# Performance work log

Hardware: AMD Instinct MI355X
Metric: run time of the kernel (lower is better)

## Reference

```python
import jax, jax.numpy as jnp
import numpy as np

TOP_K = 2

def _expert(x, w1, w2, w3):
    return (jax.nn.silu(x @ w1.T) * (x @ w3.T)) @ w2.T

def setup_inputs() -> dict:
    key = jax.random.key(0)
    ks = jax.random.split(key, 8)
    B, L, D, F, E, S = 4, 2048, 1024, 512, 16, 1
    p = lambda k, shape: (jax.random.normal(k, shape, jnp.float32) * 0.02)
    return {
        "x": jax.random.normal(ks[0], (B, L, D), jnp.float32),
        "gate_w": p(ks[1], (E, D)),
        "expert_bias": jnp.zeros((E,), jnp.float32),
        "sw1": p(ks[2], (S, F, D)),
        "sw2": p(ks[3], (S, D, F)),
        "sw3": p(ks[4], (S, F, D)),
        "ew1": p(ks[5], (E, F, D)),
        "ew2": p(ks[6], (E, D, F)),
        "ew3": p(ks[7], (E, F, D)),
    }

def reference(x, gate_w, expert_bias, sw1, sw2, sw3, ew1, ew2, ew3):
    B, L, D = x.shape
    E = gate_w.shape[0]
    flat_x = x.reshape(-1, D)  # [T, D], T = B*L

    # Shared experts (always-on)
    shared = sum(_expert(flat_x, sw1[i], sw2[i], sw3[i]) for i in range(sw1.shape[0]))

    # Router (eval mode: no jitter noise, no bias update; expert_bias buffer added)
    logits = flat_x @ gate_w.T + expert_bias          # [T, E]
    probs = jax.nn.softmax(logits, axis=-1)
    topw, topi = jax.lax.top_k(probs, TOP_K)          # [T, k]
    topw = topw / jnp.sum(topw, axis=-1, keepdims=True)

    # Routed experts: combine weight per (token, expert); zero weight => zero contribution,
    # identical math to the masked gather/scatter in the original.
    out = jnp.zeros_like(flat_x)
    for e in range(E):  # fixed small structural loop over experts
        cw = jnp.sum(jnp.where(topi == e, topw, 0.0), axis=-1)  # [T]
        out = out + cw[:, None] * _expert(flat_x, ew1[e], ew2[e], ew3[e])

    y = (shared + out).reshape(B, L, D)
    return y, probs
```

## Files before the change

kernel.cpp:

```cpp
#include <hip/hip_runtime.h>

typedef unsigned short u16;
typedef __bf16 bf16_t;
typedef bf16_t bf16x8 __attribute__((ext_vector_type(8)));
typedef float f32x4 __attribute__((ext_vector_type(4)));

#define T_TOK 8192
#define DIM   1024
#define FF    512
#define NE    16
#define RBASE_SHARED (2 * T_TOK)
#define NROWS (RBASE_SHARED + T_TOK)
#define MAXTILES 256
#define NSEG 512

__device__ __forceinline__ u16 f2bf(float f) {
  union { float f; unsigned u; } v; v.f = f;
  unsigned r = v.u + 0x7FFFu + ((v.u >> 16) & 1u);
  return (u16)(r >> 16);
}
__device__ __forceinline__ float bf2f(u16 h) {
  union { unsigned u; float f; } v; v.u = ((unsigned)h) << 16; return v.f;
}
__device__ __forceinline__ int clampi(int v, int lo, int hi) {
  return v < lo ? lo : (v > hi ? hi : v);
}

#define GLL16(g, l) __builtin_amdgcn_global_load_lds( \
    (const __attribute__((address_space(1))) void*)(g), \
    (__attribute__((address_space(3))) void*)(l), 16, 0, 0)

#define WAIT_VM_BARRIER(n) asm volatile("s_waitcnt vmcnt(" #n ")\n\ts_barrier" ::: "memory")
#define BARRIER_ONLY()     asm volatile("s_barrier" ::: "memory")
#define WAIT_LGKM0()       asm volatile("s_waitcnt lgkmcnt(0)" ::: "memory")

#define X4   2097152
#define SW4  131072
#define EW4  2097152
#define TOT4 (X4 + 3 * SW4 + 3 * EW4)

__global__ __launch_bounds__(256) void cvt_all_kernel(
    const float* __restrict__ x, const float* __restrict__ sw1,
    const float* __restrict__ sw2, const float* __restrict__ sw3,
    const float* __restrict__ ew1, const float* __restrict__ ew2,
    const float* __restrict__ ew3,
    u16* __restrict__ xb, u16* __restrict__ sw1b, u16* __restrict__ sw2b,
    u16* __restrict__ sw3b, u16* __restrict__ ew1b, u16* __restrict__ ew2b,
    u16* __restrict__ ew3b) {
  int i = blockIdx.x * 256 + threadIdx.x;
  const float* s; u16* dst; int j;
  if (i < X4)                       { s = x;   dst = xb;   j = i; }
  else if (i < X4 + SW4)            { s = sw1; dst = sw1b; j = i - X4; }
  else if (i < X4 + 2 * SW4)        { s = sw2; dst = sw2b; j = i - (X4 + SW4); }
  else if (i < X4 + 3 * SW4)        { s = sw3; dst = sw3b; j = i - (X4 + 2 * SW4); }
  else if (i < X4 + 3 * SW4 + EW4)      { s = ew1; dst = ew1b; j = i - (X4 + 3 * SW4); }
  else if (i < X4 + 3 * SW4 + 2 * EW4)  { s = ew2; dst = ew2b; j = i - (X4 + 3 * SW4 + EW4); }
  else if (i < TOT4)                    { s = ew3; dst = ew3b; j = i - (X4 + 3 * SW4 + 2 * EW4); }
  else return;
  float4 v = reinterpret_cast<const float4*>(s)[j];
  ushort4 o;
  o.x = f2bf(v.x); o.y = f2bf(v.y); o.z = f2bf(v.z); o.w = f2bf(v.w);
  reinterpret_cast<ushort4*>(dst)[j] = o;
}

__global__ __launch_bounds__(256) void router_kernel(
    const float* __restrict__ x, const float* __restrict__ gw,
    const float* __restrict__ ebias, float* __restrict__ probs,
    int* __restrict__ topi, float* __restrict__ topw, int* __restrict__ cnt_seg) {
  __shared__ int hist[16];
  int tid = threadIdx.x;
  int lane = tid & 63, w = tid >> 6;
  if (tid < 16) hist[tid] = 0;
  __syncthreads();
  const float4* gv = reinterpret_cast<const float4*>(gw);
  for (int it = 0; it < 2; ++it) {
    int t0 = blockIdx.x * 16 + (w + 4 * it) * 2;
    const float4* x0 = reinterpret_cast<const float4*>(x + (size_t)t0 * DIM);
    const float4* x1 = reinterpret_cast<const float4*>(x + (size_t)(t0 + 1) * DIM);
    float4 xa[4], xc[4];
#pragma unroll
    for (int j = 0; j < 4; ++j) { xa[j] = x0[j * 64 + lane]; xc[j] = x1[j * 64 + lane]; }
    float p0[16], p1[16];
#pragma unroll
    for (int e = 0; e < NE; ++e) {
      float s0 = 0.f, s1 = 0.f;
#pragma unroll
      for (int j = 0; j < 4; ++j) {
        float4 g = gv[e * 256 + j * 64 + lane];
        s0 += xa[j].x * g.x + xa[j].y * g.y + xa[j].z * g.z + xa[j].w * g.w;
        s1 += xc[j].x * g.x + xc[j].y * g.y + xc[j].z * g.z + xc[j].w * g.w;
      }
#pragma unroll
      for (int d = 1; d < 64; d <<= 1) { s0 += __shfl_xor(s0, d); s1 += __shfl_xor(s1, d); }
      float b = ebias[e];
      p0[e] = s0 + b; p1[e] = s1 + b;
    }
    float m0 = p0[0], m1 = p1[0];
#pragma unroll
    for (int e = 1; e < NE; ++e) { m0 = fmaxf(m0, p0[e]); m1 = fmaxf(m1, p1[e]); }
    float sum0 = 0.f, sum1 = 0.f;
#pragma unroll
    for (int e = 0; e < NE; ++e) {
      p0[e] = __expf(p0[e] - m0); sum0 += p0[e];
      p1[e] = __expf(p1[e] - m1); sum1 += p1[e];
    }
    float inv0 = 1.f / sum0, inv1 = 1.f / sum1;
#pragma unroll
    for (int e = 0; e < NE; ++e) { p0[e] *= inv0; p1[e] *= inv1; }
    if (lane == 0) {
#pragma unroll
      for (int j = 0; j < 4; ++j)
        reinterpret_cast<float4*>(probs + (size_t)t0 * NE)[j] =
            make_float4(p0[4 * j], p0[4 * j + 1], p0[4 * j + 2], p0[4 * j + 3]);
      float b1 = -1.f, b2 = -1.f; int i1 = 0, i2 = 0;
#pragma unroll
      for (int e = 0; e < NE; ++e) {
        float pe = p0[e];
        if (pe > b1) { b2 = b1; i2 = i1; b1 = pe; i1 = e; }
        else if (pe > b2) { b2 = pe; i2 = e; }
      }
      float ws = b1 + b2;
      reinterpret_cast<int2*>(topi)[t0] = make_int2(i1, i2);
      reinterpret_cast<float2*>(topw)[t0] = make_float2(b1 / ws, b2 / ws);
      atomicAdd(&hist[i1], 1); atomicAdd(&hist[i2], 1);
    }
    if (lane == 1) {
      int t1 = t0 + 1;
#pragma unroll
      for (int j = 0; j < 4; ++j)
        reinterpret_cast<float4*>(probs + (size_t)t1 * NE)[j] =
            make_float4(p1[4 * j], p1[4 * j + 1], p1[4 * j + 2], p1[4 * j + 3]);
      float b1 = -1.f, b2 = -1.f; int i1 = 0, i2 = 0;
#pragma unroll
      for (int e = 0; e < NE; ++e) {
        float pe = p1[e];
        if (pe > b1) { b2 = b1; i2 = i1; b1 = pe; i1 = e; }
        else if (pe > b2) { b2 = pe; i2 = e; }
      }
      float ws = b1 + b2;
      reinterpret_cast<int2*>(topi)[t1] = make_int2(i1, i2);
      reinterpret_cast<float2*>(topw)[t1] = make_float2(b1 / ws, b2 / ws);
      atomicAdd(&hist[i1], 1); atomicAdd(&hist[i2], 1);
    }
  }
  __syncthreads();
  if (tid < 16) cnt_seg[blockIdx.x * 16 + tid] = hist[tid];
}

__global__ __launch_bounds__(256) void scan_kernel(
    const int* __restrict__ cnt_seg, int* __restrict__ cnt, int* __restrict__ offs,
    int* __restrict__ seg_base, int2* __restrict__ tab) {
  __shared__ int chunk_sum[16][16];
  __shared__ int chunk_base[16][16];
  __shared__ int tot[16], off_s[17];
  int tid = threadIdx.x;
  int e = tid & 15, c = tid >> 4;
  int s0 = 0;
  for (int s = 0; s < 32; ++s) s0 += cnt_seg[(c * 32 + s) * 16 + e];
  chunk_sum[c][e] = s0;
  __syncthreads();
  if (tid < 16) {
    int r = 0;
    for (int c2 = 0; c2 < 16; ++c2) { chunk_base[c2][tid] = r; r += chunk_sum[c2][tid]; }
    tot[tid] = r;
  }
  __syncthreads();
  if (tid == 0) {
    int a = 0;
    for (int i = 0; i < 16; ++i) { off_s[i] = a; offs[i] = a; cnt[i] = tot[i]; a += tot[i]; }
    off_s[16] = RBASE_SHARED; offs[16] = RBASE_SHARED;
    int n = 0;
    for (int g = 0; g <= 16 && n < MAXTILES; ++g) {
      int M = (g == 16) ? T_TOK : tot[g];
      for (int m0 = 0; m0 < M && n < MAXTILES; m0 += 128) { tab[n] = make_int2(g, m0); ++n; }
    }
    for (; n < MAXTILES; ++n) tab[n] = make_int2(-1, 0);
  }
  __syncthreads();
  int r = off_s[e] + chunk_base[c][e];
  for (int s = 0; s < 32; ++s) {
    int seg = c * 32 + s;
    seg_base[seg * 16 + e] = r;
    r += cnt_seg[seg * 16 + e];
  }
}

__global__ __launch_bounds__(64) void scatter_kernel(
    const int* __restrict__ topi, const float* __restrict__ topw,
    const int* __restrict__ seg_base,
    int* __restrict__ idx, float* __restrict__ cwl, int* __restrict__ slotmap) {
  __shared__ int ti[16][2]; __shared__ float tw[16][2]; __shared__ int base[16];
  int b = blockIdx.x;
  int tid = threadIdx.x;
  if (tid < 16) {
    int t = b * 16 + tid;
    int2 pp = reinterpret_cast<const int2*>(topi)[t];
    ti[tid][0] = clampi(pp.x, 0, 15); ti[tid][1] = clampi(pp.y, 0, 15);
    float2 ww = reinterpret_cast<const float2*>(topw)[t];
    tw[tid][0] = ww.x; tw[tid][1] = ww.y;
    base[tid] = seg_base[b * 16 + tid];
  }
  __syncthreads();
  if (tid < 32) {
    int l = tid >> 1, s = tid & 1;
    int t = b * 16 + l;
    int e = ti[l][s];
    int rank = 0;
    for (int t2 = 0; t2 < 16; ++t2) {
      if (ti[t2][0] == e && (t2 < l || (t2 == l && 0 < s))) ++rank;
      if (ti[t2][1] == e && (t2 < l)) ++rank;
    }
    int slot = clampi(base[e] + rank, 0, NROWS - 1);
    idx[slot] = t; cwl[slot] = tw[l][s]; slotmap[t * 3 + s] = slot;
  } else if (tid < 48) {
    int l = tid - 32;
    int t = b * 16 + l;
    int sh = RBASE_SHARED + t;
    idx[sh] = t; cwl[sh] = 1.0f; slotmap[t * 3 + 2] = sh;
  }
}

__global__ __launch_bounds__(256) void gemm_silu_kernel(
    const u16* __restrict__ A, const u16* __restrict__ sw1b, const u16* __restrict__ sw3b,
    const u16* __restrict__ ew1b, const u16* __restrict__ ew3b, u16* __restrict__ G,
    const int2* __restrict__ tab, const int* __restrict__ offs,
    const int* __restrict__ cnt, const int* __restrict__ gidx) {
  const int K = DIM;
  int orig = blockIdx.x + gridDim.x * blockIdx.y;
  int xcd = orig & 7, q = orig >> 3;
  int tileid = xcd + 8 * (q & 31);
  int ny = q >> 5;
  int2 te = tab[tileid];
  int e = te.x;
  if (e < 0) return;
  e = clampi(e, 0, NE);
  int m0 = te.y;
  int M = (e == NE) ? T_TOK : cnt[e];
  M = clampi(M, 1, T_TOK);
  int rowbase = clampi(offs[e], 0, NROWS - 1);
  const u16* B1 = (e == NE) ? sw1b : ew1b + (size_t)e * FF * K;
  const u16* B3 = (e == NE) ? sw3b : ew3b + (size_t)e * FF * K;
  int n0 = ny * 128;

  __shared__ u16 As[2 * 4096], B1s[2 * 4096], B3s[2 * 4096];

  int tid = threadIdx.x;
  int lane = tid & 63, wv = tid >> 6;
  int srow = tid >> 2, sg = tid & 3;
  int sk0 = (sg ^ ((srow >> 1) & 3)) * 8;
  int sk1 = (sg ^ (((srow + 64) >> 1) & 3)) * 8;
  int r0 = min(m0 + srow, M - 1);
  int r1 = min(m0 + srow + 64, M - 1);
  int ga0 = clampi(gidx[clampi(rowbase + r0, 0, NROWS - 1)], 0, T_TOK - 1);
  int ga1 = clampi(gidx[clampi(rowbase + r1, 0, NROWS - 1)], 0, T_TOK - 1);
  const u16* Ap0 = A + (size_t)ga0 * K + sk0;
  const u16* Ap1 = A + (size_t)ga1 * K + sk1;
  const u16* B1p0 = B1 + (size_t)(n0 + srow) * K + sk0;
  const u16* B1p1 = B1 + (size_t)(n0 + srow + 64) * K + sk1;
  const u16* B3p0 = B3 + (size_t)(n0 + srow) * K + sk0;
  const u16* B3p1 = B3 + (size_t)(n0 + srow + 64) * K + sk1;
  int st0 = wv * 512, st1 = 2048 + wv * 512;

  int ln15 = lane & 15, qd = lane >> 4;
  int qsw = (qd ^ ((ln15 >> 1) & 3)) * 8;
  int wm = (wv >> 1) * 64, wn = (wv & 1) * 64;
  int aoff = (wm + ln15) * 32 + qsw;
  int boff = (wn + ln15) * 32 + qsw;

  f32x4 acc1[4][4] = {};
  f32x4 acc3[4][4] = {};

  const int nk = K / 32;
  GLL16(Ap0, As + st0);            GLL16(Ap1, As + st1);
  GLL16(B1p0, B1s + st0);          GLL16(B1p1, B1s + st1);
  GLL16(B3p0, B3s + st0);          GLL16(B3p1, B3s + st1);
  GLL16(Ap0 + 32, As + 4096 + st0);    GLL16(Ap1 + 32, As + 4096 + st1);
  GLL16(B1p0 + 32, B1s + 4096 + st0);  GLL16(B1p1 + 32, B1s + 4096 + st1);
  GLL16(B3p0 + 32, B3s + 4096 + st0);  GLL16(B3p1 + 32, B3s + 4096 + st1);

  for (int t = 0; t < nk - 2; ++t) {
    int cur = (t & 1) * 4096;
    WAIT_VM_BARRIER(6);
    bf16x8 af[4], b1f[4], b3f[4];
#pragma unroll
    for (int i = 0; i < 4; ++i) {
      af[i]  = *reinterpret_cast<const bf16x8*>(&As[cur + aoff + i * 512]);
      b1f[i] = *reinterpret_cast<const bf16x8*>(&B1s[cur + boff + i * 512]);
      b3f[i] = *reinterpret_cast<const bf16x8*>(&B3s[cur + boff + i * 512]);
    }
    WAIT_LGKM0();
    __builtin_amdgcn_sched_barrier(0);
    BARRIER_ONLY();
    int kt = (t + 2) * 32;
    GLL16(Ap0 + kt, As + cur + st0);     GLL16(Ap1 + kt, As + cur + st1);
    GLL16(B1p0 + kt, B1s + cur + st0);   GLL16(B1p1 + kt, B1s + cur + st1);
    GLL16(B3p0 + kt, B3s + cur + st0);   GLL16(B3p1 + kt, B3s + cur + st1);
#pragma unroll
    for (int i = 0; i < 4; ++i)
#pragma unroll
      for (int j = 0; j < 4; ++j) {
        acc1[i][j] = __builtin_amdgcn_mfma_f32_16x16x32_bf16(af[i], b1f[j], acc1[i][j], 0, 0, 0);
        acc3[i][j] = __builtin_amdgcn_mfma_f32_16x16x32_bf16(af[i], b3f[j], acc3[i][j], 0, 0, 0);
      }
  }
  {
    int cur = ((nk - 2) & 1) * 4096;
    WAIT_VM_BARRIER(6);
    bf16x8 af[4], b1f[4], b3f[4];
#pragma unroll
    for (int i = 0; i < 4; ++i) {
      af[i]  = *reinterpret_cast<const bf16x8*>(&As[cur + aoff + i * 512]);
      b1f[i] = *reinterpret_cast<const bf16x8*>(&B1s[cur + boff + i * 512]);
      b3f[i] = *reinterpret_cast<const bf16x8*>(&B3s[cur + boff + i * 512]);
    }
    WAIT_LGKM0();
    __builtin_amdgcn_sched_barrier(0);
#pragma unroll
    for (int i = 0; i < 4; ++i)
#pragma unroll
      for (int j = 0; j < 4; ++j) {
        acc1[i][j] = __builtin_amdgcn_mfma_f32_16x16x32_bf16(af[i], b1f[j], acc1[i][j], 0, 0, 0);
        acc3[i][j] = __builtin_amdgcn_mfma_f32_16x16x32_bf16(af[i], b3f[j], acc3[i][j], 0, 0, 0);
      }
  }
  {
    int cur = ((nk - 1) & 1) * 4096;
    WAIT_VM_BARRIER(0);
    bf16x8 af[4], b1f[4], b3f[4];
#pragma unroll
    for (int i = 0; i < 4; ++i) {
      af[i]  = *reinterpret_cast<const bf16x8*>(&As[cur + aoff + i * 512]);
      b1f[i] = *reinterpret_cast<const bf16x8*>(&B1s[cur + boff + i * 512]);
      b3f[i] = *reinterpret_cast<const bf16x8*>(&B3s[cur + boff + i * 512]);
    }
    WAIT_LGKM0();
    __builtin_amdgcn_sched_barrier(0);
#pragma unroll
    for (int i = 0; i < 4; ++i)
#pragma unroll
      for (int j = 0; j < 4; ++j) {
        acc1[i][j] = __builtin_amdgcn_mfma_f32_16x16x32_bf16(af[i], b1f[j], acc1[i][j], 0, 0, 0);
        acc3[i][j] = __builtin_amdgcn_mfma_f32_16x16x32_bf16(af[i], b3f[j], acc3[i][j], 0, 0, 0);
      }
  }

  int mrem = M - m0;
#pragma unroll
  for (int i = 0; i < 4; ++i)
#pragma unroll
    for (int r = 0; r < 4; ++r) {
      int ml = wm + i * 16 + qd * 4 + r;
      if (ml < mrem) {
        size_t orow = (size_t)clampi(rowbase + m0 + ml, 0, NROWS - 1);
#pragma unroll
        for (int j = 0; j < 4; ++j) {
          float z1 = acc1[i][j][r], z3 = acc3[i][j][r];
          float g = z1 / (1.f + __expf(-z1)) * z3;
          G[orow * FF + n0 + wn + j * 16 + ln15] = f2bf(g);
        }
      }
    }
}

__global__ __launch_bounds__(256) void gemm_out_kernel(
    const u16* __restrict__ Gb, const u16* __restrict__ sw2b, const u16* __restrict__ ew2b,
    u16* __restrict__ O, const int2* __restrict__ tab, const int* __restrict__ offs,
    const int* __restrict__ cnt, const float* __restrict__ cwl) {
  const int K = FF;
  int orig = blockIdx.x + gridDim.x * blockIdx.y;
  int xcd = orig & 7, q = orig >> 3;
  int tileid = xcd + 8 * (q & 31);
  int ny = q >> 5;
  int2 te = tab[tileid];
  int e = te.x;
  if (e < 0) return;
  e = clampi(e, 0, NE);
  int m0 = te.y;
  int M = (e == NE) ? T_TOK : cnt[e];
  M = clampi(M, 1, T_TOK);
  int rowbase = clampi(offs[e], 0, NROWS - 1);
  const u16* B = (e == NE) ? sw2b : ew2b + (size_t)e * DIM * K;
  int n0 = ny * 128;

  __shared__ u16 As[2 * 4096], Bs[2 * 4096];

  int tid = threadIdx.x;
  int lane = tid & 63, wv = tid >> 6;
  int srow = tid >> 2, sg = tid & 3;
  int sk0 = (sg ^ ((srow >> 1) & 3)) * 8;
  int sk1 = (sg ^ (((srow + 64) >> 1) & 3)) * 8;
  int r0 = clampi(rowbase + min(m0 + srow, M - 1), 0, NROWS - 1);
  int r1 = clampi(rowbase + min(m0 + srow + 64, M - 1), 0, NROWS - 1);
  const u16* Ap0 = Gb + (size_t)r0 * K + sk0;
  const u16* Ap1 = Gb + (size_t)r1 * K + sk1;
  const u16* Bp0 = B + (size_t)(n0 + srow) * K + sk0;
  const u16* Bp1 = B + (size_t)(n0 + srow + 64) * K + sk1;
  int st0 = wv * 512, st1 = 2048 + wv * 512;

  int ln15 = lane & 15, qd = lane >> 4;
  int qsw = (qd ^ ((ln15 >> 1) & 3)) * 8;
  int wm = (wv >> 1) * 64, wn = (wv & 1) * 64;
  int aoff = (wm + ln15) * 32 + qsw;
  int boff = (wn + ln15) * 32 + qsw;

  f32x4 acc[4][4] = {};

  const int nk = K / 32;
  GLL16(Ap0, As + st0);    GLL16(Ap1, As + st1);
  GLL16(Bp0, Bs + st0);    GLL16(Bp1, Bs + st1);
  GLL16(Ap0 + 32, As + 4096 + st0);  GLL16(Ap1 + 32, As + 4096 + st1);
  GLL16(Bp0 + 32, Bs + 4096 + st0);  GLL16(Bp1 + 32, Bs + 4096 + st1);

  for (int t = 0; t < nk - 2; ++t) {
    int cur = (t & 1) * 4096;
    WAIT_VM_BARRIER(4);
    bf16x8 af[4], bf[4];
#pragma unroll
    for (int i = 0; i < 4; ++i) {
      af[i] = *reinterpret_cast<const bf16x8*>(&As[cur + aoff + i * 512]);
      bf[i] = *reinterpret_cast<const bf16x8*>(&Bs[cur + boff + i * 512]);
    }
    WAIT_LGKM0();
    __builtin_amdgcn_sched_barrier(0);
    BARRIER_ONLY();
    int kt = (t + 2) * 32;
    GLL16(Ap0 + kt, As + cur + st0);   GLL16(Ap1 + kt, As + cur + st1);
    GLL16(Bp0 + kt, Bs + cur + st0);   GLL16(Bp1 + kt, Bs + cur + st1);
#pragma unroll
    for (int i = 0; i < 4; ++i)
#pragma unroll
      for (int j = 0; j < 4; ++j)
        acc[i][j] = __builtin_amdgcn_mfma_f32_16x16x32_bf16(af[i], bf[j], acc[i][j], 0, 0, 0);
  }
  {
    int cur = ((nk - 2) & 1) * 4096;
    WAIT_VM_BARRIER(4);
    bf16x8 af[4], bf[4];
#pragma unroll
    for (int i = 0; i < 4; ++i) {
      af[i] = *reinterpret_cast<const bf16x8*>(&As[cur + aoff + i * 512]);
      bf[i] = *reinterpret_cast<const bf16x8*>(&Bs[cur + boff + i * 512]);
    }
    WAIT_LGKM0();
    __builtin_amdgcn_sched_barrier(0);
#pragma unroll
    for (int i = 0; i < 4; ++i)
#pragma unroll
      for (int j = 0; j < 4; ++j)
        acc[i][j] = __builtin_amdgcn_mfma_f32_16x16x32_bf16(af[i], bf[j], acc[i][j], 0, 0, 0);
  }
  {
    int cur = ((nk - 1) & 1) * 4096;
    WAIT_VM_BARRIER(0);
    bf16x8 af[4], bf[4];
#pragma unroll
    for (int i = 0; i < 4; ++i) {
      af[i] = *reinterpret_cast<const bf16x8*>(&As[cur + aoff + i * 512]);
      bf[i] = *reinterpret_cast<const bf16x8*>(&Bs[cur + boff + i * 512]);
    }
    WAIT_LGKM0();
    __builtin_amdgcn_sched_barrier(0);
#pragma unroll
    for (int i = 0; i < 4; ++i)
#pragma unroll
      for (int j = 0; j < 4; ++j)
        acc[i][j] = __builtin_amdgcn_mfma_f32_16x16x32_bf16(af[i], bf[j], acc[i][j], 0, 0, 0);
  }

  int mrem = M - m0;
#pragma unroll
  for (int i = 0; i < 4; ++i)
#pragma unroll
    for (int r = 0; r < 4; ++r) {
      int ml = wm + i * 16 + qd * 4 + r;
      if (ml < mrem) {
        int slot = clampi(rowbase + m0 + ml, 0, NROWS - 1);
        float cw = cwl[slot];
#pragma unroll
        for (int j = 0; j < 4; ++j)
          O[(size_t)slot * DIM + n0 + wn + j * 16 + ln15] = f2bf(acc[i][j][r] * cw);
      }
    }
}

__global__ __launch_bounds__(256) void combine_kernel(
    const u16* __restrict__ O, const int* __restrict__ slotmap, float* __restrict__ y) {
  int t = blockIdx.x;
  int c = threadIdx.x;
  int s0 = clampi(slotmap[t * 3], 0, NROWS - 1);
  int s1 = clampi(slotmap[t * 3 + 1], 0, NROWS - 1);
  int s2 = clampi(slotmap[t * 3 + 2], 0, NROWS - 1);
  ushort4 a = reinterpret_cast<const ushort4*>(O + (size_t)s0 * DIM)[c];
  ushort4 b = reinterpret_cast<const ushort4*>(O + (size_t)s1 * DIM)[c];
  ushort4 d = reinterpret_cast<const ushort4*>(O + (size_t)s2 * DIM)[c];
  float4 r;
  r.x = bf2f(a.x) + bf2f(b.x) + bf2f(d.x);
  r.y = bf2f(a.y) + bf2f(b.y) + bf2f(d.y);
  r.z = bf2f(a.z) + bf2f(b.z) + bf2f(d.z);
  r.w = bf2f(a.w) + bf2f(b.w) + bf2f(d.w);
  reinterpret_cast<float4*>(y + (size_t)t * DIM)[c] = r;
}

extern "C" void kernel_launch(void* const* d_in, const int* in_sizes, int n_in,
                              void* d_out, int out_size, void* d_ws, size_t ws_size,
                              hipStream_t stream) {
  const float* x     = (const float*)d_in[0];
  const float* gw    = (const float*)d_in[1];
  const float* ebias = (const float*)d_in[2];
  const float* sw1   = (const float*)d_in[3];
  const float* sw2   = (const float*)d_in[4];
  const float* sw3   = (const float*)d_in[5];
  const float* ew1   = (const float*)d_in[6];
  const float* ew2   = (const float*)d_in[7];
  const float* ew3   = (const float*)d_in[8];
  float* y = (float*)d_out;
  float* probs = y + (size_t)T_TOK * DIM;

  char* ws = (char*)d_ws;
  size_t o = 0;
  auto alloc = [&](size_t bytes) -> char* {
    char* p = ws + o;
    o = (o + bytes + 255) & ~(size_t)255;
    return p;
  };
  u16* G    = (u16*)alloc((size_t)NROWS * FF * 2);
  u16* sw1b = (u16*)alloc((size_t)FF * DIM * 2);
  u16* sw2b = (u16*)alloc((size_t)FF * DIM * 2);
  u16* sw3b = (u16*)alloc((size_t)FF * DIM * 2);
  u16* ew2b = (u16*)alloc((size_t)NE * FF * DIM * 2);
  char* aliasBase = alloc((size_t)NROWS * DIM * 2);
  u16* xb   = (u16*)aliasBase;
  u16* ew1b = (u16*)(aliasBase + (size_t)T_TOK * DIM * 2);
  u16* ew3b = (u16*)(aliasBase + (size_t)T_TOK * DIM * 2 + (size_t)NE * FF * DIM * 2);
  u16* O    = (u16*)aliasBase;
  int*   topi    = (int*)alloc(T_TOK * 2 * 4);
  float* topw    = (float*)alloc(T_TOK * 2 * 4);
  int*   idx     = (int*)alloc(NROWS * 4);
  float* cwl     = (float*)alloc(NROWS * 4);
  int*   slotmap = (int*)alloc(T_TOK * 3 * 4);
  int2*  tab     = (int2*)alloc(MAXTILES * 8);
  int*   cnt_seg = (int*)alloc(NSEG * 16 * 4);
  int*   seg_base= (int*)alloc(NSEG * 16 * 4);
  int*   cnt     = (int*)alloc(256);
  int*   offs    = (int*)alloc(256);

  router_kernel<<<NSEG, 256, 0, stream>>>(x, gw, ebias, probs, topi, topw, cnt_seg);
  scan_kernel<<<1, 256, 0, stream>>>(cnt_seg, cnt, offs, seg_base, tab);
  scatter_kernel<<<NSEG, 64, 0, stream>>>(topi, topw, seg_base, idx, cwl, slotmap);
  cvt_all_kernel<<<TOT4 / 256, 256, 0, stream>>>(x, sw1, sw2, sw3, ew1, ew2, ew3,
                                                 xb, sw1b, sw2b, sw3b, ew1b, ew2b, ew3b);

  gemm_silu_kernel<<<dim3(MAXTILES, 4, 1), 256, 0, stream>>>(
      xb, sw1b, sw3b, ew1b, ew3b, G, tab, offs, cnt, idx);
  gemm_out_kernel<<<dim3(MAXTILES, 8, 1), 256, 0, stream>>>(
      G, sw2b, ew2b, O, tab, offs, cnt, cwl);
  combine_kernel<<<T_TOK, 256, 0, stream>>>(O, slotmap, y);
}
```

Baseline: 443.7 us.

## Triple-buffer down-proj GEMM, add MFMA priority, stagger tile order, unroll K loops

The down-projection GEMM now uses a three-stage LDS ring. The next prefetch is issued right after the wait and goes into a buffer no wave is reading, so the per-iteration barrier before the loads is dropped. Both grouped GEMMs raise wave priority around MFMA blocks, fully unroll their K loops with constant buffer offsets, and use a 1D grid whose tile index is rotated per N-slice. The rotation spreads concurrently running blocks across different expert tiles. The extra LDS raises shared memory per block, which may reduce occupancy, and the removed barrier depends on the three-stage ring being race-free.

```diff
diff --git a/kernel.cpp b/kernel.cpp
--- a/kernel.cpp
+++ b/kernel.cpp
@@ -226,10 +226,11 @@
     const int2* __restrict__ tab, const int* __restrict__ offs,
     const int* __restrict__ cnt, const int* __restrict__ gidx) {
   const int K = DIM;
-  int orig = blockIdx.x + gridDim.x * blockIdx.y;
-  int xcd = orig & 7, q = orig >> 3;
-  int tileid = xcd + 8 * (q & 31);
-  int ny = q >> 5;
+  int orig = blockIdx.x;
+  int xcd = orig & 7, r = orig >> 3;
+  int cc = r & 31, s = r >> 5;
+  int tileid = xcd + 8 * ((cc + 9 * s) & 31);
+  int ny = s;
   int2 te = tab[tileid];
   int e = te.x;
   if (e < 0) return;
@@ -270,7 +271,6 @@
   f32x4 acc1[4][4] = {};
   f32x4 acc3[4][4] = {};
 
-  const int nk = K / 32;
   GLL16(Ap0, As + st0);            GLL16(Ap1, As + st1);
   GLL16(B1p0, B1s + st0);          GLL16(B1p1, B1s + st1);
   GLL16(B3p0, B3s + st0);          GLL16(B3p1, B3s + st1);
@@ -278,8 +278,9 @@
   GLL16(B1p0 + 32, B1s + 4096 + st0);  GLL16(B1p1 + 32, B1s + 4096 + st1);
   GLL16(B3p0 + 32, B3s + 4096 + st0);  GLL16(B3p1 + 32, B3s + 4096 + st1);
 
-  for (int t = 0; t < nk - 2; ++t) {
-    int cur = (t & 1) * 4096;
+#pragma unroll
+  for (int t = 0; t < 30; ++t) {
+    const int cur = (t & 1) * 4096;
     WAIT_VM_BARRIER(6);
     bf16x8 af[4], b1f[4], b3f[4];
 #pragma unroll
@@ -291,10 +292,11 @@
     WAIT_LGKM0();
     __builtin_amdgcn_sched_barrier(0);
     BARRIER_ONLY();
-    int kt = (t + 2) * 32;
+    const int kt = (t + 2) * 32;
     GLL16(Ap0 + kt, As + cur + st0);     GLL16(Ap1 + kt, As + cur + st1);
     GLL16(B1p0 + kt, B1s + cur + st0);   GLL16(B1p1 + kt, B1s + cur + st1);
     GLL16(B3p0 + kt, B3s + cur + st0);   GLL16(B3p1 + kt, B3s + cur + st1);
+    __builtin_amdgcn_s_setprio(1);
 #pragma unroll
     for (int i = 0; i < 4; ++i)
 #pragma unroll
@@ -302,9 +304,10 @@
         acc1[i][j] = __builtin_amdgcn_mfma_f32_16x16x32_bf16(af[i], b1f[j], acc1[i][j], 0, 0, 0);
         acc3[i][j] = __builtin_amdgcn_mfma_f32_16x16x32_bf16(af[i], b3f[j], acc3[i][j], 0, 0, 0);
       }
+    __builtin_amdgcn_s_setprio(0);
   }
   {
-    int cur = ((nk - 2) & 1) * 4096;
+    const int cur = 0;
     WAIT_VM_BARRIER(6);
     bf16x8 af[4], b1f[4], b3f[4];
 #pragma unroll
@@ -315,6 +318,7 @@
     }
     WAIT_LGKM0();
     __builtin_amdgcn_sched_barrier(0);
+    __builtin_amdgcn_s_setprio(1);
 #pragma unroll
     for (int i = 0; i < 4; ++i)
 #pragma unroll
@@ -322,9 +326,10 @@
         acc1[i][j] = __builtin_amdgcn_mfma_f32_16x16x32_bf16(af[i], b1f[j], acc1[i][j], 0, 0, 0);
         acc3[i][j] = __builtin_amdgcn_mfma_f32_16x16x32_bf16(af[i], b3f[j], acc3[i][j], 0, 0, 0);
       }
+    __builtin_amdgcn_s_setprio(0);
   }
   {
-    int cur = ((nk - 1) & 1) * 4096;
+    const int cur = 4096;
     WAIT_VM_BARRIER(0);
     bf16x8 af[4], b1f[4], b3f[4];
 #pragma unroll
@@ -335,6 +340,7 @@
     }
     WAIT_LGKM0();
     __builtin_amdgcn_sched_barrier(0);
+    __builtin_amdgcn_s_setprio(1);
 #pragma unroll
     for (int i = 0; i < 4; ++i)
 #pragma unroll
@@ -342,19 +348,20 @@
         acc1[i][j] = __builtin_amdgcn_mfma_f32_16x16x32_bf16(af[i], b1f[j], acc1[i][j], 0, 0, 0);
         acc3[i][j] = __builtin_amdgcn_mfma_f32_16x16x32_bf16(af[i], b3f[j], acc3[i][j], 0, 0, 0);
       }
+    __builtin_amdgcn_s_setprio(0);
   }
 
   int mrem = M - m0;
 #pragma unroll
   for (int i = 0; i < 4; ++i)
 #pragma unroll
-    for (int r = 0; r < 4; ++r) {
-      int ml = wm + i * 16 + qd * 4 + r;
+    for (int r2 = 0; r2 < 4; ++r2) {
+      int ml = wm + i * 16 + qd * 4 + r2;
       if (ml < mrem) {
         size_t orow = (size_t)clampi(rowbase + m0 + ml, 0, NROWS - 1);
 #pragma unroll
         for (int j = 0; j < 4; ++j) {
-          float z1 = acc1[i][j][r], z3 = acc3[i][j][r];
+          float z1 = acc1[i][j][r2], z3 = acc3[i][j][r2];
           float g = z1 / (1.f + __expf(-z1)) * z3;
           G[orow * FF + n0 + wn + j * 16 + ln15] = f2bf(g);
         }
@@ -367,10 +374,11 @@
     u16* __restrict__ O, const int2* __restrict__ tab, const int* __restrict__ offs,
     const int* __restrict__ cnt, const float* __restrict__ cwl) {
   const int K = FF;
-  int orig = blockIdx.x + gridDim.x * blockIdx.y;
-  int xcd = orig & 7, q = orig >> 3;
-  int tileid = xcd + 8 * (q & 31);
-  int ny = q >> 5;
+  int orig = blockIdx.x;
+  int xcd = orig & 7, r = orig >> 3;
+  int cc = r & 31, s = r >> 5;
+  int tileid = xcd + 8 * ((cc + 9 * s) & 31);
+  int ny = s;
   int2 te = tab[tileid];
   int e = te.x;
   if (e < 0) return;
@@ -382,7 +390,7 @@
   const u16* B = (e == NE) ? sw2b : ew2b + (size_t)e * DIM * K;
   int n0 = ny * 128;
 
-  __shared__ u16 As[2 * 4096], Bs[2 * 4096];
+  __shared__ u16 As[3 * 4096], Bs[3 * 4096];
 
   int tid = threadIdx.x;
   int lane = tid & 63, wv = tid >> 6;
@@ -405,15 +413,19 @@
 
   f32x4 acc[4][4] = {};
 
-  const int nk = K / 32;
   GLL16(Ap0, As + st0);    GLL16(Ap1, As + st1);
   GLL16(Bp0, Bs + st0);    GLL16(Bp1, Bs + st1);
   GLL16(Ap0 + 32, As + 4096 + st0);  GLL16(Ap1 + 32, As + 4096 + st1);
   GLL16(Bp0 + 32, Bs + 4096 + st0);  GLL16(Bp1 + 32, Bs + 4096 + st1);
 
-  for (int t = 0; t < nk - 2; ++t) {
-    int cur = (t & 1) * 4096;
+#pragma unroll
+  for (int t = 0; t < 14; ++t) {
+    const int cur = (t % 3) * 4096;
+    const int nxt = ((t + 2) % 3) * 4096;
     WAIT_VM_BARRIER(4);
+    const int kt = (t + 2) * 32;
+    GLL16(Ap0 + kt, As + nxt + st0);   GLL16(Ap1 + kt, As + nxt + st1);
+    GLL16(Bp0 + kt, Bs + nxt + st0);   GLL16(Bp1 + kt, Bs + nxt + st1);
     bf16x8 af[4], bf[4];
 #pragma unroll
     for (int i = 0; i < 4; ++i) {
@@ -422,18 +434,16 @@
     }
     WAIT_LGKM0();
     __builtin_amdgcn_sched_barrier(0);
-    BARRIER_ONLY();
-    int kt = (t + 2) * 32;
-    GLL16(Ap0 + kt, As + cur + st0);   GLL16(Ap1 + kt, As + cur + st1);
-    GLL16(Bp0 + kt, Bs + cur + st0);   GLL16(Bp1 + kt, Bs + cur + st1);
+    __builtin_amdgcn_s_setprio(1);
 #pragma unroll
     for (int i = 0; i < 4; ++i)
 #pragma unroll
       for (int j = 0; j < 4; ++j)
         acc[i][j] = __builtin_amdgcn_mfma_f32_16x16x32_bf16(af[i], bf[j], acc[i][j], 0, 0, 0);
+    __builtin_amdgcn_s_setprio(0);
   }
   {
-    int cur = ((nk - 2) & 1) * 4096;
+    const int cur = (14 % 3) * 4096;
     WAIT_VM_BARRIER(4);
     bf16x8 af[4], bf[4];
 #pragma unroll
@@ -443,14 +453,16 @@
     }
     WAIT_LGKM0();
     __builtin_amdgcn_sched_barrier(0);
+    __builtin_amdgcn_s_setprio(1);
 #pragma unroll
     for (int i = 0; i < 4; ++i)
 #pragma unroll
       for (int j = 0; j < 4; ++j)
         acc[i][j] = __builtin_amdgcn_mfma_f32_16x16x32_bf16(af[i], bf[j], acc[i][j], 0, 0, 0);
+    __builtin_amdgcn_s_setprio(0);
   }
   {
-    int cur = ((nk - 1) & 1) * 4096;
+    const int cur = (15 % 3) * 4096;
     WAIT_VM_BARRIER(0);
     bf16x8 af[4], bf[4];
 #pragma unroll
@@ -460,25 +472,27 @@
     }
     WAIT_LGKM0();
     __builtin_amdgcn_sched_barrier(0);
+    __builtin_amdgcn_s_setprio(1);
 #pragma unroll
     for (int i = 0; i < 4; ++i)
 #pragma unroll
       for (int j = 0; j < 4; ++j)
         acc[i][j] = __builtin_amdgcn_mfma_f32_16x16x32_bf16(af[i], bf[j], acc[i][j], 0, 0, 0);
+    __builtin_amdgcn_s_setprio(0);
   }
 
   int mrem = M - m0;
 #pragma unroll
   for (int i = 0; i < 4; ++i)
 #pragma unroll
-    for (int r = 0; r < 4; ++r) {
-      int ml = wm + i * 16 + qd * 4 + r;
+    for (int r2 = 0; r2 < 4; ++r2) {
+      int ml = wm + i * 16 + qd * 4 + r2;
       if (ml < mrem) {
         int slot = clampi(rowbase + m0 + ml, 0, NROWS - 1);
         float cw = cwl[slot];
 #pragma unroll
         for (int j = 0; j < 4; ++j)
-          O[(size_t)slot * DIM + n0 + wn + j * 16 + ln15] = f2bf(acc[i][j][r] * cw);
+          O[(size_t)slot * DIM + n0 + wn + j * 16 + ln15] = f2bf(acc[i][j][r2] * cw);
       }
     }
 }
@@ -550,9 +564,9 @@
   cvt_all_kernel<<<TOT4 / 256, 256, 0, stream>>>(x, sw1, sw2, sw3, ew1, ew2, ew3,
                                                  xb, sw1b, sw2b, sw3b, ew1b, ew2b, ew3b);
 
-  gemm_silu_kernel<<<dim3(MAXTILES, 4, 1), 256, 0, stream>>>(
+  gemm_silu_kernel<<<1024, 256, 0, stream>>>(
       xb, sw1b, sw3b, ew1b, ew3b, G, tab, offs, cnt, idx);
-  gemm_out_kernel<<<dim3(MAXTILES, 8, 1), 256, 0, stream>>>(
+  gemm_out_kernel<<<2048, 256, 0, stream>>>(
       G, sw2b, ew2b, O, tab, offs, cnt, cwl);
   combine_kernel<<<T_TOK, 256, 0, stream>>>(O, slotmap, y);
 }
```

Measured after the change: 416.0 us. -6.2%, faster.
